# Kernel tuning notes

Hardware: AMD Instinct MI355X
Metric: run time of the kernel (lower is better)

Reference implementation:

```python
import jax, jax.numpy as jnp
import numpy as np

B, L, F = 4, 8192, 1024
H, D = 16, 64
EPS = 1e-6

def _phi(x):
    # ELU+1 positive feature map, standard for linear attention
    return jax.nn.elu(x) + 1.0

def setup_inputs() -> dict:
    key = jax.random.key(0)
    ks = jax.random.split(key, 6)
    s_in = 1.0
    s_w = 1.0 / np.sqrt(F)
    s_o = 1.0 / np.sqrt(H * D)
    return {
        "inputs_q": jax.random.normal(ks[0], (B, L, F), jnp.float32),
        "inputs_kv": jax.random.normal(ks[1], (B, L, F), jnp.float32),
        "Wq": jax.random.normal(ks[2], (F, H, D), jnp.float32) * s_w,
        "Wk": jax.random.normal(ks[3], (F, H, D), jnp.float32) * s_w,
        "Wv": jax.random.normal(ks[4], (F, H, D), jnp.float32) * s_w,
        "Wo": jax.random.normal(ks[5], (H, D, F), jnp.float32) * s_o,
    }

def reference(inputs_q, inputs_kv, Wq, Wk, Wv, Wo):
    # QKV projections (split-head kernels, no bias)
    q = jnp.einsum('bqf,fhd->bqhd', inputs_q, Wq)   # [B,Lq,H,D]
    k = jnp.einsum('bkf,fhd->bkhd', inputs_kv, Wk)  # [B,Lk,H,D]
    v = jnp.einsum('bkf,fhd->bkhd', inputs_kv, Wv)  # [B,Lk,H,D]

    qp = _phi(q)
    kp = _phi(k)

    # Linear attention: O = phi(q) @ (phi(k)^T V) / (phi(q) . sum_k phi(k))
    kv = jnp.einsum('bkhd,bkhe->bhde', kp, v)       # [B,H,D,D] small state
    ksum = jnp.sum(kp, axis=1)                       # [B,H,D]
    z = 1.0 / (jnp.einsum('bqhd,bhd->bqh', qp, ksum) + EPS)
    out = jnp.einsum('bqhd,bhde,bqh->bqhe', qp, kv, z)  # [B,Lq,H,D]

    # Output projection
    return jnp.einsum('bqhe,hef->bqf', out, Wo)      # [B,Lq,F]
```

## Files before the change

kernel.cpp:

```cpp
#include <hip/hip_runtime.h>
#include <hip/hip_fp16.h>
#include <math.h>

typedef _Float16 half8  __attribute__((ext_vector_type(8)));
typedef _Float16 half4v __attribute__((ext_vector_type(4)));
typedef float    floatx4 __attribute__((ext_vector_type(4)));

#define NB   4
#define LL   8192
#define FF   1024
#define HH   16
#define DD   64
#define MTOT 32768
#define KK   1024
#define NN   1024
#define ZSCALE 65536.0f

__device__ __forceinline__ void gload_lds16(const void* g, void* l) {
  __builtin_amdgcn_global_load_lds(
      (const __attribute__((address_space(1))) void*)g,
      (__attribute__((address_space(3))) void*)l, 16, 0, 0);
}

__device__ __forceinline__ float phi_act(float x) {
  return x > 0.f ? x + 1.f : __expf(x);
}

__global__ void k_cvt2(const float* __restrict__ a, const float* __restrict__ b,
                       _Float16* __restrict__ da, _Float16* __restrict__ db, int n4each) {
  int stride = gridDim.x * blockDim.x;
  for (int i = blockIdx.x * blockDim.x + threadIdx.x; i < 2 * n4each; i += stride) {
    const float* s; _Float16* d; int j;
    if (i < n4each) { s = a; d = da; j = i; }
    else            { s = b; d = db; j = i - n4each; }
    float4 v = reinterpret_cast<const float4*>(s)[j];
    half4v h;
    h[0] = (_Float16)v.x; h[1] = (_Float16)v.y; h[2] = (_Float16)v.z; h[3] = (_Float16)v.w;
    reinterpret_cast<half4v*>(d)[j] = h;
  }
}

__global__ void k_cvt(const float* __restrict__ src, _Float16* __restrict__ dst, int n4) {
  int stride = gridDim.x * blockDim.x;
  for (int i = blockIdx.x * blockDim.x + threadIdx.x; i < n4; i += stride) {
    float4 v = reinterpret_cast<const float4*>(src)[i];
    half4v h;
    h[0] = (_Float16)v.x; h[1] = (_Float16)v.y; h[2] = (_Float16)v.z; h[3] = (_Float16)v.w;
    reinterpret_cast<half4v*>(dst)[i] = h;
  }
}

__global__ void k_cvt_t(const float* __restrict__ W0, const float* __restrict__ W1,
                        const float* __restrict__ W2,
                        _Float16* __restrict__ T0, _Float16* __restrict__ TKV) {
  __shared__ float tile[32][33];
  int bid = blockIdx.x;
  int w = bid >> 10, rem = bid & 1023;
  int ti = rem >> 5, tj = rem & 31;
  const float* src = (w == 0) ? W0 : (w == 1) ? W1 : W2;
  int t = threadIdx.x;
  int r = t >> 3, c4 = (t & 7) << 2;
  float4 v = *reinterpret_cast<const float4*>(&src[(size_t)(ti * 32 + r) * FF + tj * 32 + c4]);
  tile[r][c4 + 0] = v.x; tile[r][c4 + 1] = v.y; tile[r][c4 + 2] = v.z; tile[r][c4 + 3] = v.w;
  __syncthreads();
  half4v h;
  h[0] = (_Float16)tile[c4 + 0][r];
  h[1] = (_Float16)tile[c4 + 1][r];
  h[2] = (_Float16)tile[c4 + 2][r];
  h[3] = (_Float16)tile[c4 + 3][r];
  int n = tj * 32 + r;
  _Float16* dst; size_t orow;
  if (w == 0) { dst = T0;  orow = n; }
  else        { dst = TKV; orow = (size_t)(n >> 6) * 128 + (n & 63) + (w == 2 ? 64 : 0); }
  *reinterpret_cast<half4v*>(&dst[orow * FF + ti * 32 + c4]) = h;
}


template<int MATB, int HALF>
__device__ __forceinline__ void stage_half(const _Float16* __restrict__ G, int row0,
                                           int col0, _Float16* plane, int tid) {
  #pragma unroll
  for (int is = 0; is < 2; ++is) {
    int lin = is * 8192 + tid * 16;
    int swz = lin ^ (((lin >> 7) & 7) << 4);
    int rp = swz >> 7;
    int kb = swz & 127;
    int row;
    if constexpr (MATB) row = (rp >> 5) * 64 + HALF * 32 + (rp & 31);
    else                row = (rp >> 6) * 128 + HALF * 64 + (rp & 63);
    gload_lds16(G + (size_t)(row0 + row) * 1024 + col0 + (kb >> 1),
                (char*)plane + lin);
  }
}

__device__ __forceinline__ half8 frag_read(const _Float16* plane, int rp, int kk, int lh) {
  int byte = rp * 128 + kk * 64 + lh * 16;
  byte ^= ((byte >> 7) & 7) << 4;
  return *(const half8*)((const char*)plane + byte);
}

template<int MH, int NH>
__device__ __forceinline__ void qreads(const _Float16* sm, int buf,
                                       half8 (&bA)[8], half8 (&bB)[2][4],
                                       int wr, int wc, int lr, int lh) {
  if constexpr (NH == 0) {
    const _Float16* Ap = sm + buf * 32768 + MH * 8192;
    #pragma unroll
    for (int m = 0; m < 4; ++m)
      #pragma unroll
      for (int kk = 0; kk < 2; ++kk)
        bA[m * 2 + kk] = frag_read(Ap, wr * 64 + m * 16 + lr, kk, lh);
  }
  if constexpr (MH == 0) {
    const _Float16* Bp = sm + buf * 32768 + 16384 + NH * 8192;
    #pragma unroll
    for (int n = 0; n < 2; ++n)
      #pragma unroll
      for (int kk = 0; kk < 2; ++kk)
        bB[NH][n * 2 + kk] = frag_read(Bp, wc * 32 + n * 16 + lr, kk, lh);
  }
}

template<int MH, int NH, bool VM4>
__device__ __forceinline__ void qmfma(half8 (&bA)[8], half8 (&bB)[2][4],
                                      floatx4 (&acc)[8][4]) {
  if constexpr (VM4) {
    asm volatile("s_waitcnt vmcnt(4)" ::: "memory");
  }
  __builtin_amdgcn_s_barrier();
  __builtin_amdgcn_s_setprio(1);
  #pragma unroll
  for (int m = 0; m < 4; ++m)
    #pragma unroll
    for (int n = 0; n < 2; ++n)
      #pragma unroll
      for (int kk = 0; kk < 2; ++kk)
        acc[MH * 4 + m][NH * 2 + n] = __builtin_amdgcn_mfma_f32_16x16x32_f16(
            bA[m * 2 + kk], bB[NH][n * 2 + kk], acc[MH * 4 + m][NH * 2 + n], 0, 0, 0);
  __builtin_amdgcn_s_setprio(0);
  __builtin_amdgcn_s_barrier();
}

template<int TBUF>
__device__ __forceinline__ void do_tile(int t, const _Float16* __restrict__ Ab,
                                        const _Float16* __restrict__ Bb,
                                        int i0, int j0, _Float16* sm, int tid,
                                        half8 (&bA)[8], half8 (&bB)[2][4],
                                        floatx4 (&acc)[8][4],
                                        int wr, int wc, int lr, int lh) {
  _Float16* self  = sm + TBUF * 32768;
  _Float16* other = sm + (TBUF ^ 1) * 32768;
  const int c1 = ((t + 1 < 16) ? (t + 1) : 15) * 64;
  const int c2 = ((t + 2 < 16) ? (t + 2) : 15) * 64;
  qreads<0, 0>(sm, TBUF, bA, bB, wr, wc, lr, lh);
  stage_half<1, 1>(Bb, j0, c1, other + 24576, tid);
  qmfma<0, 0, false>(bA, bB, acc);
  qreads<0, 1>(sm, TBUF, bA, bB, wr, wc, lr, lh);
  stage_half<0, 1>(Ab, i0, c1, other + 8192, tid);
  qmfma<0, 1, false>(bA, bB, acc);
  qreads<1, 0>(sm, TBUF, bA, bB, wr, wc, lr, lh);
  stage_half<0, 0>(Ab, i0, c2, self + 0, tid);
  qmfma<1, 0, false>(bA, bB, acc);
  stage_half<1, 0>(Bb, j0, c2, self + 16384, tid);
  qmfma<1, 1, true>(bA, bB, acc);
}

template<int MODE, bool PHI>
__global__ __launch_bounds__(512, 2)
void k_gemm(const _Float16* __restrict__ A, const _Float16* __restrict__ BT,
            void* __restrict__ Cptr, float* __restrict__ aux, float* __restrict__ aux2,
            float outScale) {
  __shared__ __align__(16) _Float16 smem[65536];
  const int tid  = threadIdx.x;
  const int lane = tid & 63;
  const int wid  = tid >> 6;
  const int wr = wid >> 2, wc = wid & 3;
  const int lr = lane & 15, lh = lane >> 4;

  constexpr int NT = (MODE == 1) ? 8 : 4;
  constexpr int CH = (MODE == 1) ? 128 : 64;
  const int tile = (blockIdx.x & 7) * CH + (blockIdx.x >> 3);
  const int tm = tile / NT, tn = tile % NT;
  const int i0 = tm * 256, j0 = tn * 256;

  const _Float16* Ab = A;
  const _Float16* Bb = (MODE == 2) ? BT + ((size_t)(i0 >> 13)) * ((size_t)NN * KK) : BT;

  floatx4 acc[8][4];
  #pragma unroll
  for (int m = 0; m < 8; ++m)
    #pragma unroll
    for (int n = 0; n < 4; ++n)
      #pragma unroll
      for (int r = 0; r < 4; ++r) acc[m][n][r] = 0.f;

  _Float16* sm = (_Float16*)smem;
  half8 bA[8];
  half8 bB[2][4];

  stage_half<0, 0>(Ab, i0, 0,  sm + 0,             tid);
  stage_half<1, 0>(Bb, j0, 0,  sm + 16384,         tid);
  stage_half<1, 1>(Bb, j0, 0,  sm + 24576,         tid);
  stage_half<0, 1>(Ab, i0, 0,  sm + 8192,          tid);
  stage_half<0, 0>(Ab, i0, 64, sm + 32768 + 0,     tid);
  stage_half<1, 0>(Bb, j0, 64, sm + 32768 + 16384, tid);
  asm volatile("s_waitcnt vmcnt(4)" ::: "memory");
  __builtin_amdgcn_s_barrier();

  #pragma unroll 1
  for (int tt = 0; tt < 8; ++tt) {
    do_tile<0>(2 * tt,     Ab, Bb, i0, j0, sm, tid, bA, bB, acc, wr, wc, lr, lh);
    do_tile<1>(2 * tt + 1, Ab, Bb, i0, j0, sm, tid, bA, bB, acc, wr, wc, lr, lh);
  }

  asm volatile("s_waitcnt vmcnt(0)" ::: "memory");
  __builtin_amdgcn_s_barrier();

  if constexpr (MODE == 0) {
    _Float16* C = (_Float16*)Cptr;
    const int bq = i0 >> 13;
    float ks[4];
    #pragma unroll
    for (int n = 0; n < 4; ++n)
      ks[n] = aux[(size_t)bq * 1024 + j0 + wc * 64 + n * 16 + lr];
    #pragma unroll
    for (int m = 0; m < 8; ++m) {
      int row = i0 + wr * 128 + m * 16 + lh * 4;
      #pragma unroll
      for (int r = 0; r < 4; ++r) {
        float p[4];
        float dot = 0.f;
        #pragma unroll
        for (int n = 0; n < 4; ++n) {
          p[n] = phi_act(acc[m][n][r]);
          dot = fmaf(p[n], ks[n], dot);
        }
        dot += __shfl_xor(dot, 1);
        dot += __shfl_xor(dot, 2);
        dot += __shfl_xor(dot, 4);
        dot += __shfl_xor(dot, 8);
        float zf = ZSCALE / (dot + 1e-6f);
        #pragma unroll
        for (int n = 0; n < 4; ++n)
          C[(size_t)(row + r) * NN + j0 + wc * 64 + n * 16 + lr] = (_Float16)(p[n] * zf);
      }
    }
  } else if constexpr (MODE == 2) {
    float* C = (float*)Cptr;
    #pragma unroll
    for (int m = 0; m < 8; ++m) {
      int row = i0 + wr * 128 + m * 16 + lh * 4;
      #pragma unroll
      for (int n = 0; n < 4; ++n) {
        int col = j0 + wc * 64 + n * 16 + lr;
        #pragma unroll
        for (int r = 0; r < 4; ++r)
          C[(size_t)(row + r) * NN + col] = acc[m][n][r] * outScale;
      }
    }
  } else {
    const int b  = i0 >> 13;
    const int l0 = i0 & 8191;
    const int isK = !(wc & 1);
    const int hh  = tn * 2 + (wc >> 1);
    float s[4] = {0.f, 0.f, 0.f, 0.f};
    #pragma unroll
    for (int m = 0; m < 8; ++m) {
      int l0l = wr * 128 + m * 16 + lh * 4;
      #pragma unroll
      for (int n = 0; n < 4; ++n) {
        int n_loc = wc * 64 + n * 16 + lr;
        int byte = (n_loc * 512 + l0l * 2) ^ ((n_loc & 7) << 4);
        half4v h;
        #pragma unroll
        for (int r = 0; r < 4; ++r) {
          float v = acc[m][n][r];
          if (isK) { v = phi_act(v); s[n] += v; }
          h[r] = (_Float16)v;
        }
        *(half4v*)((char*)sm + byte) = h;
      }
    }
    if (isK) {
      #pragma unroll
      for (int n = 0; n < 4; ++n) {
        s[n] += __shfl_xor(s[n], 16);
        s[n] += __shfl_xor(s[n], 32);
      }
      if (lh == 0) {
        int ch = (l0 >> 7) + wr;
        size_t base = ((size_t)b * 64 + ch) * 1024 + (size_t)hh * 64 + lr;
        #pragma unroll
        for (int n = 0; n < 4; ++n) aux[base + n * 16] = s[n];
      }
    }
    __syncthreads();
    const int khd = wid >> 2;
    const int db = ((wid >> 1) & 1) * 32, eb = (wid & 1) * 32;
    const int hb = khd * 128;
    floatx4 a2[2][2];
    #pragma unroll
    for (int md = 0; md < 2; ++md)
      #pragma unroll
      for (int ne = 0; ne < 2; ++ne)
        #pragma unroll
        for (int r = 0; r < 4; ++r) a2[md][ne][r] = 0.f;
    #pragma unroll 1
    for (int ks2 = 0; ks2 < 8; ++ks2) {
      half8 af[2], bf[2];
      #pragma unroll
      for (int md = 0; md < 2; ++md) {
        int n_loc = hb + db + md * 16 + lr;
        int byte = (n_loc * 512 + ks2 * 64 + lh * 16) ^ ((n_loc & 7) << 4);
        af[md] = *(const half8*)((const char*)sm + byte);
      }
      #pragma unroll
      for (int ne = 0; ne < 2; ++ne) {
        int n_loc = hb + 64 + eb + ne * 16 + lr;
        int byte = (n_loc * 512 + ks2 * 64 + lh * 16) ^ ((n_loc & 7) << 4);
        bf[ne] = *(const half8*)((const char*)sm + byte);
      }
      #pragma unroll
      for (int md = 0; md < 2; ++md)
        #pragma unroll
        for (int ne = 0; ne < 2; ++ne)
          a2[md][ne] = __builtin_amdgcn_mfma_f32_16x16x32_f16(af[md], bf[ne], a2[md][ne], 0, 0, 0);
    }
    const int lch = l0 >> 8;
    float* op = aux2 + ((((size_t)b * 16 + tn * 2 + khd) * 32) + lch) * 4096;
    #pragma unroll
    for (int md = 0; md < 2; ++md)
      #pragma unroll
      for (int ne = 0; ne < 2; ++ne)
        #pragma unroll
        for (int r = 0; r < 4; ++r)
          op[(db + md * 16 + lh * 4 + r) * 64 + eb + ne * 16 + lr] = a2[md][ne][r];
  }
}

__global__ void k_ksum_red(const float* __restrict__ part, float* __restrict__ ksum) {
  int i = blockIdx.x * 256 + threadIdx.x;
  int b = i >> 10, col = i & 1023;
  float s = 0.f;
  for (int c = 0; c < 64; ++c) s += part[((size_t)b * 64 + c) * 1024 + col];
  ksum[i] = s;
}

__global__ void k_reduce_kv(const float* __restrict__ kvpart, float* __restrict__ kv) {
  int gid = blockIdx.x * 256 + threadIdx.x;
  int bh = gid >> 12, i = gid & 4095;
  float s = 0.f;
  for (int c = 0; c < 32; ++c) s += kvpart[((size_t)bh * 32 + c) * 4096 + i];
  kv[gid] = s;
}

__global__ __launch_bounds__(256)
void k_mker(const float* __restrict__ kv, const _Float16* __restrict__ Wo16,
            _Float16* __restrict__ MT) {
  __shared__ float kvs[4096];
  int bid = blockIdx.x;
  int fc = bid & 3, h = (bid >> 2) & 15, b = bid >> 6;
  const float* kvp = kv + ((size_t)b * 16 + h) * 4096;
  for (int i = threadIdx.x; i < 4096; i += 256) kvs[i] = kvp[i];
  __syncthreads();
  int f = fc * 256 + threadIdx.x;
  float acc[64];
  #pragma unroll
  for (int d = 0; d < 64; ++d) acc[d] = 0.f;
  for (int e = 0; e < 64; ++e) {
    float wv = (float)Wo16[(size_t)(h * 64 + e) * 1024 + f];
    #pragma unroll
    for (int d = 0; d < 64; ++d) acc[d] = fmaf(kvs[d * 64 + e], wv, acc[d]);
  }
  _Float16* op = MT + ((size_t)b * 1024 + f) * 1024 + h * 64;
  #pragma unroll
  for (int g = 0; g < 8; ++g) {
    half8 o;
    #pragma unroll
    for (int j = 0; j < 8; ++j) o[j] = (_Float16)acc[g * 8 + j];
    *(half8*)&op[g * 8] = o;
  }
}

extern "C" void kernel_launch(void* const* d_in, const int* in_sizes, int n_in,
                              void* d_out, int out_size, void* d_ws, size_t ws_size,
                              hipStream_t stream) {
  (void)in_sizes; (void)n_in; (void)out_size; (void)ws_size;
  const float* xq  = (const float*)d_in[0];
  const float* xkv = (const float*)d_in[1];
  const float* Wq  = (const float*)d_in[2];
  const float* Wk  = (const float*)d_in[3];
  const float* Wv  = (const float*)d_in[4];
  const float* Wo  = (const float*)d_in[5];

  char* ws = (char*)d_ws;
  _Float16* qp16   = (_Float16*)(ws + 0);
  float*    kvpart = (float*)(ws + 67108864);
  float*    ksum_part = (float*)(ws + 100663296);
  float*    ksum   = (float*)(ws + 101711872);
  float*    kv     = (float*)(ws + 101728256);
  _Float16* WqT    = (_Float16*)(ws + 102776832);
  _Float16* WKV    = (_Float16*)(ws + 104873984);
  _Float16* Wo16   = (_Float16*)(ws + 109068288);
  _Float16* MT     = (_Float16*)(ws + 111165440);

  _Float16* Xq16  = (_Float16*)d_out;
  _Float16* Xkv16 = Xq16 + 33554432;

  k_cvt2<<<4096, 256, 0, stream>>>(xq, xkv, Xq16, Xkv16, 8388608);
  k_cvt<<<512,  256, 0, stream>>>(Wo, Wo16, 262144);
  k_cvt_t<<<3072, 256, 0, stream>>>(Wq, Wk, Wv, WqT, WKV);

  k_gemm<1, false><<<1024, 512, 0, stream>>>(Xkv16, WKV, nullptr, ksum_part, kvpart, 1.0f);
  k_ksum_red<<<16, 256, 0, stream>>>(ksum_part, ksum);
  k_reduce_kv<<<1024, 256, 0, stream>>>(kvpart, kv);
  k_mker<<<256, 256, 0, stream>>>(kv, Wo16, MT);

  k_gemm<0, true><<<512, 512, 0, stream>>>(Xq16, WqT, qp16, ksum, nullptr, 1.0f);

  k_gemm<2, false><<<512, 512, 0, stream>>>(qp16, MT, d_out, nullptr, nullptr, 1.0f / ZSCALE);
}
```

Baseline: 429.8 us.

## Shrink GEMM block tiles to 128x128 with 4 waves and more blocks

```diff
diff --git a/kernel.cpp b/kernel.cpp
--- a/kernel.cpp
+++ b/kernel.cpp
@@ -76,18 +76,16 @@
 }
 
 
-template<int MATB, int HALF>
+template<int HALF>
 __device__ __forceinline__ void stage_half(const _Float16* __restrict__ G, int row0,
                                            int col0, _Float16* plane, int tid) {
   #pragma unroll
   for (int is = 0; is < 2; ++is) {
-    int lin = is * 8192 + tid * 16;
+    int lin = is * 4096 + tid * 16;
     int swz = lin ^ (((lin >> 7) & 7) << 4);
     int rp = swz >> 7;
     int kb = swz & 127;
-    int row;
-    if constexpr (MATB) row = (rp >> 5) * 64 + HALF * 32 + (rp & 31);
-    else                row = (rp >> 6) * 128 + HALF * 64 + (rp & 63);
+    int row = (rp >> 5) * 64 + HALF * 32 + (rp & 31);
     gload_lds16(G + (size_t)(row0 + row) * 1024 + col0 + (kb >> 1),
                 (char*)plane + lin);
   }
@@ -101,18 +99,18 @@
 
 template<int MH, int NH>
 __device__ __forceinline__ void qreads(const _Float16* sm, int buf,
-                                       half8 (&bA)[8], half8 (&bB)[2][4],
+                                       half8 (&bA)[4], half8 (&bB)[2][4],
                                        int wr, int wc, int lr, int lh) {
   if constexpr (NH == 0) {
-    const _Float16* Ap = sm + buf * 32768 + MH * 8192;
-    #pragma unroll
-    for (int m = 0; m < 4; ++m)
+    const _Float16* Ap = sm + buf * 16384 + MH * 4096;
+    #pragma unroll
+    for (int m = 0; m < 2; ++m)
       #pragma unroll
       for (int kk = 0; kk < 2; ++kk)
-        bA[m * 2 + kk] = frag_read(Ap, wr * 64 + m * 16 + lr, kk, lh);
+        bA[m * 2 + kk] = frag_read(Ap, wr * 32 + m * 16 + lr, kk, lh);
   }
   if constexpr (MH == 0) {
-    const _Float16* Bp = sm + buf * 32768 + 16384 + NH * 8192;
+    const _Float16* Bp = sm + buf * 16384 + 8192 + NH * 4096;
     #pragma unroll
     for (int n = 0; n < 2; ++n)
       #pragma unroll
@@ -122,21 +120,21 @@
 }
 
 template<int MH, int NH, bool VM4>
-__device__ __forceinline__ void qmfma(half8 (&bA)[8], half8 (&bB)[2][4],
-                                      floatx4 (&acc)[8][4]) {
+__device__ __forceinline__ void qmfma(half8 (&bA)[4], half8 (&bB)[2][4],
+                                      floatx4 (&acc)[4][4]) {
   if constexpr (VM4) {
     asm volatile("s_waitcnt vmcnt(4)" ::: "memory");
   }
   __builtin_amdgcn_s_barrier();
   __builtin_amdgcn_s_setprio(1);
   #pragma unroll
-  for (int m = 0; m < 4; ++m)
+  for (int m = 0; m < 2; ++m)
     #pragma unroll
     for (int n = 0; n < 2; ++n)
       #pragma unroll
       for (int kk = 0; kk < 2; ++kk)
-        acc[MH * 4 + m][NH * 2 + n] = __builtin_amdgcn_mfma_f32_16x16x32_f16(
-            bA[m * 2 + kk], bB[NH][n * 2 + kk], acc[MH * 4 + m][NH * 2 + n], 0, 0, 0);
+        acc[MH * 2 + m][NH * 2 + n] = __builtin_amdgcn_mfma_f32_16x16x32_f16(
+            bA[m * 2 + kk], bB[NH][n * 2 + kk], acc[MH * 2 + m][NH * 2 + n], 0, 0, 0);
   __builtin_amdgcn_s_setprio(0);
   __builtin_amdgcn_s_barrier();
 }
@@ -145,65 +143,65 @@
 __device__ __forceinline__ void do_tile(int t, const _Float16* __restrict__ Ab,
                                         const _Float16* __restrict__ Bb,
                                         int i0, int j0, _Float16* sm, int tid,
-                                        half8 (&bA)[8], half8 (&bB)[2][4],
-                                        floatx4 (&acc)[8][4],
+                                        half8 (&bA)[4], half8 (&bB)[2][4],
+                                        floatx4 (&acc)[4][4],
                                         int wr, int wc, int lr, int lh) {
-  _Float16* self  = sm + TBUF * 32768;
-  _Float16* other = sm + (TBUF ^ 1) * 32768;
+  _Float16* self  = sm + TBUF * 16384;
+  _Float16* other = sm + (TBUF ^ 1) * 16384;
   const int c1 = ((t + 1 < 16) ? (t + 1) : 15) * 64;
   const int c2 = ((t + 2 < 16) ? (t + 2) : 15) * 64;
   qreads<0, 0>(sm, TBUF, bA, bB, wr, wc, lr, lh);
-  stage_half<1, 1>(Bb, j0, c1, other + 24576, tid);
+  stage_half<1>(Bb, j0, c1, other + 12288, tid);
   qmfma<0, 0, false>(bA, bB, acc);
   qreads<0, 1>(sm, TBUF, bA, bB, wr, wc, lr, lh);
-  stage_half<0, 1>(Ab, i0, c1, other + 8192, tid);
+  stage_half<1>(Ab, i0, c1, other + 4096, tid);
   qmfma<0, 1, false>(bA, bB, acc);
   qreads<1, 0>(sm, TBUF, bA, bB, wr, wc, lr, lh);
-  stage_half<0, 0>(Ab, i0, c2, self + 0, tid);
+  stage_half<0>(Ab, i0, c2, self + 0, tid);
   qmfma<1, 0, false>(bA, bB, acc);
-  stage_half<1, 0>(Bb, j0, c2, self + 16384, tid);
+  stage_half<0>(Bb, j0, c2, self + 8192, tid);
   qmfma<1, 1, true>(bA, bB, acc);
 }
 
 template<int MODE, bool PHI>
-__global__ __launch_bounds__(512, 2)
+__global__ __launch_bounds__(256, 2)
 void k_gemm(const _Float16* __restrict__ A, const _Float16* __restrict__ BT,
             void* __restrict__ Cptr, float* __restrict__ aux, float* __restrict__ aux2,
             float outScale) {
-  __shared__ __align__(16) _Float16 smem[65536];
+  __shared__ __align__(16) _Float16 smem[32768];
   const int tid  = threadIdx.x;
   const int lane = tid & 63;
   const int wid  = tid >> 6;
-  const int wr = wid >> 2, wc = wid & 3;
+  const int wr = wid >> 1, wc = wid & 1;
   const int lr = lane & 15, lh = lane >> 4;
 
-  constexpr int NT = (MODE == 1) ? 8 : 4;
-  constexpr int CH = (MODE == 1) ? 128 : 64;
+  constexpr int NT = (MODE == 1) ? 16 : 8;
+  constexpr int CH = (MODE == 1) ? 512 : 256;
   const int tile = (blockIdx.x & 7) * CH + (blockIdx.x >> 3);
   const int tm = tile / NT, tn = tile % NT;
-  const int i0 = tm * 256, j0 = tn * 256;
+  const int i0 = tm * 128, j0 = tn * 128;
 
   const _Float16* Ab = A;
   const _Float16* Bb = (MODE == 2) ? BT + ((size_t)(i0 >> 13)) * ((size_t)NN * KK) : BT;
 
-  floatx4 acc[8][4];
+  floatx4 acc[4][4];
   #pragma unroll
-  for (int m = 0; m < 8; ++m)
+  for (int m = 0; m < 4; ++m)
     #pragma unroll
     for (int n = 0; n < 4; ++n)
       #pragma unroll
       for (int r = 0; r < 4; ++r) acc[m][n][r] = 0.f;
 
   _Float16* sm = (_Float16*)smem;
-  half8 bA[8];
+  half8 bA[4];
   half8 bB[2][4];
 
-  stage_half<0, 0>(Ab, i0, 0,  sm + 0,             tid);
-  stage_half<1, 0>(Bb, j0, 0,  sm + 16384,         tid);
-  stage_half<1, 1>(Bb, j0, 0,  sm + 24576,         tid);
-  stage_half<0, 1>(Ab, i0, 0,  sm + 8192,          tid);
-  stage_half<0, 0>(Ab, i0, 64, sm + 32768 + 0,     tid);
-  stage_half<1, 0>(Bb, j0, 64, sm + 32768 + 16384, tid);
+  stage_half<0>(Ab, i0, 0,  sm + 0,            tid);
+  stage_half<0>(Bb, j0, 0,  sm + 8192,         tid);
+  stage_half<1>(Bb, j0, 0,  sm + 12288,        tid);
+  stage_half<1>(Ab, i0, 0,  sm + 4096,         tid);
+  stage_half<0>(Ab, i0, 64, sm + 16384,        tid);
+  stage_half<0>(Bb, j0, 64, sm + 16384 + 8192, tid);
   asm volatile("s_waitcnt vmcnt(4)" ::: "memory");
   __builtin_amdgcn_s_barrier();
 
@@ -224,8 +222,8 @@
     for (int n = 0; n < 4; ++n)
       ks[n] = aux[(size_t)bq * 1024 + j0 + wc * 64 + n * 16 + lr];
     #pragma unroll
-    for (int m = 0; m < 8; ++m) {
-      int row = i0 + wr * 128 + m * 16 + lh * 4;
+    for (int m = 0; m < 4; ++m) {
+      int row = i0 + wr * 64 + m * 16 + lh * 4;
       #pragma unroll
       for (int r = 0; r < 4; ++r) {
         float p[4];
@@ -248,8 +246,8 @@
   } else if constexpr (MODE == 2) {
     float* C = (float*)Cptr;
     #pragma unroll
-    for (int m = 0; m < 8; ++m) {
-      int row = i0 + wr * 128 + m * 16 + lh * 4;
+    for (int m = 0; m < 4; ++m) {
+      int row = i0 + wr * 64 + m * 16 + lh * 4;
       #pragma unroll
       for (int n = 0; n < 4; ++n) {
         int col = j0 + wc * 64 + n * 16 + lr;
@@ -261,16 +259,16 @@
   } else {
     const int b  = i0 >> 13;
     const int l0 = i0 & 8191;
-    const int isK = !(wc & 1);
-    const int hh  = tn * 2 + (wc >> 1);
+    const int isK = (wc == 0);
+    char* smb = (char*)smem;
     float s[4] = {0.f, 0.f, 0.f, 0.f};
     #pragma unroll
-    for (int m = 0; m < 8; ++m) {
-      int l0l = wr * 128 + m * 16 + lh * 4;
+    for (int m = 0; m < 4; ++m) {
+      int l0l = wr * 64 + m * 16 + lh * 4;
       #pragma unroll
       for (int n = 0; n < 4; ++n) {
         int n_loc = wc * 64 + n * 16 + lr;
-        int byte = (n_loc * 512 + l0l * 2) ^ ((n_loc & 7) << 4);
+        int byte = (n_loc * 256 + l0l * 2) ^ ((n_loc & 7) << 4);
         half4v h;
         #pragma unroll
         for (int r = 0; r < 4; ++r) {
@@ -278,7 +276,7 @@
           if (isK) { v = phi_act(v); s[n] += v; }
           h[r] = (_Float16)v;
         }
-        *(half4v*)((char*)sm + byte) = h;
+        *(half4v*)(smb + byte) = h;
       }
     }
     if (isK) {
@@ -288,16 +286,14 @@
         s[n] += __shfl_xor(s[n], 32);
       }
       if (lh == 0) {
-        int ch = (l0 >> 7) + wr;
-        size_t base = ((size_t)b * 64 + ch) * 1024 + (size_t)hh * 64 + lr;
+        int ch = (l0 >> 6) + wr;
+        size_t base = ((size_t)b * 128 + ch) * 1024 + (size_t)tn * 64 + lr;
         #pragma unroll
         for (int n = 0; n < 4; ++n) aux[base + n * 16] = s[n];
       }
     }
     __syncthreads();
-    const int khd = wid >> 2;
-    const int db = ((wid >> 1) & 1) * 32, eb = (wid & 1) * 32;
-    const int hb = khd * 128;
+    const int db = (wid >> 1) * 32, eb = (wid & 1) * 32;
     floatx4 a2[2][2];
     #pragma unroll
     for (int md = 0; md < 2; ++md)
@@ -306,19 +302,19 @@
         #pragma unroll
         for (int r = 0; r < 4; ++r) a2[md][ne][r] = 0.f;
     #pragma unroll 1
-    for (int ks2 = 0; ks2 < 8; ++ks2) {
+    for (int ks2 = 0; ks2 < 4; ++ks2) {
       half8 af[2], bf[2];
       #pragma unroll
       for (int md = 0; md < 2; ++md) {
-        int n_loc = hb + db + md * 16 + lr;
-        int byte = (n_loc * 512 + ks2 * 64 + lh * 16) ^ ((n_loc & 7) << 4);
-        af[md] = *(const half8*)((const char*)sm + byte);
+        int n_loc = db + md * 16 + lr;
+        int byte = (n_loc * 256 + ks2 * 64 + lh * 16) ^ ((n_loc & 7) << 4);
+        af[md] = *(const half8*)(smb + byte);
       }
       #pragma unroll
       for (int ne = 0; ne < 2; ++ne) {
-        int n_loc = hb + 64 + eb + ne * 16 + lr;
-        int byte = (n_loc * 512 + ks2 * 64 + lh * 16) ^ ((n_loc & 7) << 4);
-        bf[ne] = *(const half8*)((const char*)sm + byte);
+        int n_loc = 64 + eb + ne * 16 + lr;
+        int byte = (n_loc * 256 + ks2 * 64 + lh * 16) ^ ((n_loc & 7) << 4);
+        bf[ne] = *(const half8*)(smb + byte);
       }
       #pragma unroll
       for (int md = 0; md < 2; ++md)
@@ -326,8 +322,8 @@
         for (int ne = 0; ne < 2; ++ne)
           a2[md][ne] = __builtin_amdgcn_mfma_f32_16x16x32_f16(af[md], bf[ne], a2[md][ne], 0, 0, 0);
     }
-    const int lch = l0 >> 8;
-    float* op = aux2 + ((((size_t)b * 16 + tn * 2 + khd) * 32) + lch) * 4096;
+    const int lch = l0 >> 7;
+    float* op = aux2 + (((size_t)b * 16 + tn) * 64 + lch) * 4096;
     #pragma unroll
     for (int md = 0; md < 2; ++md)
       #pragma unroll
@@ -342,7 +338,7 @@
   int i = blockIdx.x * 256 + threadIdx.x;
   int b = i >> 10, col = i & 1023;
   float s = 0.f;
-  for (int c = 0; c < 64; ++c) s += part[((size_t)b * 64 + c) * 1024 + col];
+  for (int c = 0; c < 128; ++c) s += part[((size_t)b * 128 + c) * 1024 + col];
   ksum[i] = s;
 }
 
@@ -350,7 +346,7 @@
   int gid = blockIdx.x * 256 + threadIdx.x;
   int bh = gid >> 12, i = gid & 4095;
   float s = 0.f;
-  for (int c = 0; c < 32; ++c) s += kvpart[((size_t)bh * 32 + c) * 4096 + i];
+  for (int c = 0; c < 64; ++c) s += kvpart[((size_t)bh * 64 + c) * 4096 + i];
   kv[gid] = s;
 }
 
@@ -396,13 +392,13 @@
   char* ws = (char*)d_ws;
   _Float16* qp16   = (_Float16*)(ws + 0);
   float*    kvpart = (float*)(ws + 67108864);
-  float*    ksum_part = (float*)(ws + 100663296);
-  float*    ksum   = (float*)(ws + 101711872);
-  float*    kv     = (float*)(ws + 101728256);
-  _Float16* WqT    = (_Float16*)(ws + 102776832);
-  _Float16* WKV    = (_Float16*)(ws + 104873984);
-  _Float16* Wo16   = (_Float16*)(ws + 109068288);
-  _Float16* MT     = (_Float16*)(ws + 111165440);
+  float*    ksum_part = (float*)(ws + 134217728);
+  float*    ksum   = (float*)(ws + 136314880);
+  float*    kv     = (float*)(ws + 136331264);
+  _Float16* WqT    = (_Float16*)(ws + 137379840);
+  _Float16* WKV    = (_Float16*)(ws + 139476992);
+  _Float16* Wo16   = (_Float16*)(ws + 143671296);
+  _Float16* MT     = (_Float16*)(ws + 145768448);
 
   _Float16* Xq16  = (_Float16*)d_out;
   _Float16* Xkv16 = Xq16 + 33554432;
@@ -411,12 +407,12 @@
   k_cvt<<<512,  256, 0, stream>>>(Wo, Wo16, 262144);
   k_cvt_t<<<3072, 256, 0, stream>>>(Wq, Wk, Wv, WqT, WKV);
 
-  k_gemm<1, false><<<1024, 512, 0, stream>>>(Xkv16, WKV, nullptr, ksum_part, kvpart, 1.0f);
+  k_gemm<1, false><<<4096, 256, 0, stream>>>(Xkv16, WKV, nullptr, ksum_part, kvpart, 1.0f);
   k_ksum_red<<<16, 256, 0, stream>>>(ksum_part, ksum);
   k_reduce_kv<<<1024, 256, 0, stream>>>(kvpart, kv);
   k_mker<<<256, 256, 0, stream>>>(kv, Wo16, MT);
 
-  k_gemm<0, true><<<512, 512, 0, stream>>>(Xq16, WqT, qp16, ksum, nullptr, 1.0f);
-
-  k_gemm<2, false><<<512, 512, 0, stream>>>(qp16, MT, d_out, nullptr, nullptr, 1.0f / ZSCALE);
-}
+  k_gemm<0, true><<<2048, 256, 0, stream>>>(Xq16, WqT, qp16, ksum, nullptr, 1.0f);
+
+  k_gemm<2, false><<<2048, 256, 0, stream>>>(qp16, MT, d_out, nullptr, nullptr, 1.0f / ZSCALE);
+}
```

After: 490.6 us. +14.1%, slower.
